# Kernel optimization log

Hardware: AMD Instinct MI355X
Metric: run time of the kernel (lower is better)

The kernel has to match this reference:

```python
import jax, jax.numpy as jnp
import numpy as np

B, S, D, H, L = 4, 2048, 512, 8, 4
DFF = 4 * D
CW = 128          # context_window
LS_MIN, LS_MAX = -6.0, 1.5


def setup_inputs() -> dict:
    key = jax.random.key(0)
    ks = jax.random.split(key, 10)
    s = 0.02
    p = lambda k, shape: jax.random.normal(k, shape, jnp.float32) * s
    return {
        "x": jax.random.normal(ks[0], (B, S, 2), jnp.float32),
        "W_in": p(ks[1], (D, 2)), "b_in": jnp.zeros((D,), jnp.float32),
        "pos": p(ks[2], (1, S, D)),
        "Wqkv": p(ks[3], (L, 3 * D, D)), "bqkv": jnp.zeros((L, 3 * D), jnp.float32),
        "Wo": p(ks[4], (L, D, D)), "bo": jnp.zeros((L, D), jnp.float32),
        "W1": p(ks[5], (L, DFF, D)), "b1": jnp.zeros((L, DFF), jnp.float32),
        "W2": p(ks[6], (L, D, DFF)), "b2": jnp.zeros((L, D), jnp.float32),
        "ln1_g": jnp.ones((L, D), jnp.float32), "ln1_b": jnp.zeros((L, D), jnp.float32),
        "ln2_g": jnp.ones((L, D), jnp.float32), "ln2_b": jnp.zeros((L, D), jnp.float32),
        "W_head": p(ks[7], (4, D)), "b_head": jnp.zeros((4,), jnp.float32),
    }


def _ln(x, g, b):
    m = x.mean(-1, keepdims=True)
    v = ((x - m) ** 2).mean(-1, keepdims=True)
    return (x - m) / jnp.sqrt(v + 1e-5) * g + b


def reference(x, W_in, b_in, pos, Wqkv, bqkv, Wo, bo, W1, b1, W2, b2,
              ln1_g, ln1_b, ln2_g, ln2_b, W_head, b_head):
    Bx, Sx, _ = x.shape
    h = x @ W_in.T + b_in + pos[:, :Sx, :]          # [B,S,D]
    idx = jnp.arange(Sx)
    # True = disallowed: future OR older than context window
    mask = (idx[None, :] > idx[:, None]) | (idx[None, :] < idx[:, None] - CW)
    dh = D // H
    scale = 1.0 / np.sqrt(dh).astype(np.float32)
    neg = jnp.float32(-1e30)
    for l in range(L):
        # self-attention (post-LN, as nn.TransformerEncoderLayer default)
        qkv = h @ Wqkv[l].T + bqkv[l]               # [B,S,3D]
        q, k, v = jnp.split(qkv, 3, axis=-1)
        q = q.reshape(Bx, Sx, H, dh)
        k = k.reshape(Bx, Sx, H, dh)
        v = v.reshape(Bx, Sx, H, dh)
        scores = jnp.einsum('bqhd,bkhd->bhqk', q, k) * scale
        scores = jnp.where(mask, neg, scores)
        attn = jax.nn.softmax(scores, axis=-1)
        o = jnp.einsum('bhqk,bkhd->bqhd', attn, v).reshape(Bx, Sx, D)
        h = _ln(h + o @ Wo[l].T + bo[l], ln1_g[l], ln1_b[l])
        # GELU FFN (exact erf gelu, torch default)
        ff = jax.nn.gelu(h @ W1[l].T + b1[l], approximate=False) @ W2[l].T + b2[l]
        h = _ln(h + ff, ln2_g[l], ln2_b[l])
    out = h @ W_head.T + b_head                     # [B,S,4]
    mu = out[..., :2]
    log_sigma = jnp.clip(out[..., 2:], LS_MIN, LS_MAX)
    return mu, log_sigma
```

## Files before the change

kernel.cpp:

```cpp
#include <hip/hip_runtime.h>
#include <hip/hip_bf16.h>
#include <math.h>

constexpr int Bc = 4;
constexpr int Sc = 2048;
constexpr int Dc = 512;
constexpr int Hc = 8;
constexpr int DHc = 64;
constexpr int Lc = 4;
constexpr int DFFc = 2048;
constexpr int Tc = Bc * Sc;
constexpr int QKVW = 3 * Dc;

typedef __attribute__((ext_vector_type(8))) short short8;
typedef __attribute__((ext_vector_type(4))) float f32x4;

static __device__ __forceinline__ float u16tof(unsigned int u) {
  return __uint_as_float(u << 16);
}
static __device__ __forceinline__ unsigned short ftobf(float f) {
  __hip_bfloat16 h = __float2bfloat16(f);
  return *reinterpret_cast<unsigned short*>(&h);
}
static __device__ __forceinline__ void gload_lds16(const void* g, void* l) {
  __builtin_amdgcn_global_load_lds(
      (const __attribute__((address_space(1))) void*)g,
      (__attribute__((address_space(3))) void*)l, 16, 0, 0);
}

static __device__ __forceinline__ int swzK(int row, int col) {
  return row * 64 + ((((col >> 3) ^ (row & 7)) << 3) | (col & 7));
}
static __device__ __forceinline__ int swzW(int row, int col) {
  return row * 192 + ((((col >> 3) ^ (row & 7)) << 3) | (col & 7));
}

__global__ __launch_bounds__(256) void k_f2bf(const float* __restrict__ in,
                                              unsigned short* __restrict__ out,
                                              int n) {
  int i = blockIdx.x * 256 + threadIdx.x;
  if (i < n) out[i] = ftobf(in[i]);
}

__global__ __launch_bounds__(256) void k_embed(const float* __restrict__ x,
                                               const float* __restrict__ W_in,
                                               const float* __restrict__ b_in,
                                               const float* __restrict__ pos,
                                               float* __restrict__ h,
                                               unsigned short* __restrict__ hb) {
  int idx = blockIdx.x * 256 + threadIdx.x;
  int t = idx >> 9;
  int d = idx & 511;
  int s = t & (Sc - 1);
  float v = x[t * 2 + 0] * W_in[d * 2 + 0] + x[t * 2 + 1] * W_in[d * 2 + 1] +
            b_in[d] + pos[(size_t)s * Dc + d];
  h[idx] = v;
  hb[idx] = ftobf(v);
}

template <int MODE, int OUTBF, int KK>
__global__ __launch_bounds__(256) void k_mgemm(const unsigned short* __restrict__ A,
                                               const unsigned short* __restrict__ W,
                                               const float* __restrict__ bias,
                                               const float* __restrict__ res,
                                               void* __restrict__ Cout,
                                               int M, int N) {
  constexpr int NSTEP = KK / 32;
  __shared__ short As[4][512 * 8];
  __shared__ short Bs[4][512 * 8];
  const int tid = threadIdx.x;
  const int lane = tid & 63;
  const int wid = tid >> 6;
  const int wm = wid >> 1;
  const int wn = wid & 1;

  const int nwg = gridDim.x * gridDim.y;
  const int bid = blockIdx.y * gridDim.x + blockIdx.x;
  const int swz = (bid & 7) * (nwg >> 3) + (bid >> 3);
  const int m0 = (swz / gridDim.x) * 128;
  const int n0 = (swz % gridDim.x) * 128;

  int r0S, c0S, r1S, c1S;
  {
    int p = tid;
    int rp = p >> 3, q = (p & 7) ^ (rp & 7);
    r0S = (rp << 1) | (q >> 2);
    c0S = q & 3;
    p = tid + 256;
    rp = p >> 3;
    q = (p & 7) ^ (rp & 7);
    r1S = (rp << 1) | (q >> 2);
    c1S = q & 3;
  }
  const unsigned short* a0p = A + (size_t)(m0 + r0S) * KK + c0S * 8;
  const unsigned short* a1p = A + (size_t)(m0 + r1S) * KK + c1S * 8;
  const unsigned short* b0p = W + (size_t)(n0 + r0S) * KK + c0S * 8;
  const unsigned short* b1p = W + (size_t)(n0 + r1S) * KK + c1S * 8;
  const int d0 = (tid & ~63) * 8;
  const int d1 = ((tid + 256) & ~63) * 8;

  f32x4 acc[4][4] = {};
  const int lr = lane & 15;
  const int chr = lane >> 4;

#pragma unroll
  for (int t = 0; t < 3; ++t) {
    const int ko = t * 32;
    gload_lds16(a0p + ko, &As[t][d0]);
    gload_lds16(a1p + ko, &As[t][d1]);
    gload_lds16(b0p + ko, &Bs[t][d0]);
    gload_lds16(b1p + ko, &Bs[t][d1]);
  }

#pragma unroll 4
  for (int s = 0; s < NSTEP; ++s) {
    if (s + 3 <= NSTEP)
      asm volatile("s_waitcnt vmcnt(8)" ::: "memory");
    else if (s + 2 <= NSTEP)
      asm volatile("s_waitcnt vmcnt(4)" ::: "memory");
    else
      asm volatile("s_waitcnt vmcnt(0)" ::: "memory");
    __builtin_amdgcn_s_barrier();
    __builtin_amdgcn_sched_barrier(0);

    if (s + 3 < NSTEP) {
      const int ko = (s + 3) * 32;
      const int nb = (s + 3) & 3;
      gload_lds16(a0p + ko, &As[nb][d0]);
      gload_lds16(a1p + ko, &As[nb][d1]);
      gload_lds16(b0p + ko, &Bs[nb][d0]);
      gload_lds16(b1p + ko, &Bs[nb][d1]);
    }

    const int buf = s & 3;
    short8 af[4], bfr[4];
#pragma unroll
    for (int mi = 0; mi < 4; ++mi) {
      int row = wm * 64 + mi * 16 + lr;
      int rp = row >> 1;
      int p = rp * 8 + (((((row & 1) << 2) | chr)) ^ (rp & 7));
      af[mi] = *(const short8*)&As[buf][p * 8];
    }
#pragma unroll
    for (int ni = 0; ni < 4; ++ni) {
      int row = wn * 64 + ni * 16 + lr;
      int rp = row >> 1;
      int p = rp * 8 + (((((row & 1) << 2) | chr)) ^ (rp & 7));
      bfr[ni] = *(const short8*)&Bs[buf][p * 8];
    }
    __builtin_amdgcn_s_setprio(1);
#pragma unroll
    for (int mi = 0; mi < 4; ++mi)
#pragma unroll
      for (int ni = 0; ni < 4; ++ni)
        acc[mi][ni] = __builtin_amdgcn_mfma_f32_16x16x32_bf16(
            af[mi], bfr[ni], acc[mi][ni], 0, 0, 0);
    __builtin_amdgcn_s_setprio(0);
  }

  const int cj = lane & 15;
  const int rj = (lane >> 4) * 4;
#pragma unroll
  for (int mi = 0; mi < 4; ++mi) {
#pragma unroll
    for (int ni = 0; ni < 4; ++ni) {
      int n = n0 + wn * 64 + ni * 16 + cj;
      float bn = bias[n];
#pragma unroll
      for (int j = 0; j < 4; ++j) {
        int m = m0 + wm * 64 + mi * 16 + rj + j;
        float v = acc[mi][ni][j] + bn;
        if (MODE == 1) v += res[(size_t)m * N + n];
        if (MODE == 2) v = 0.5f * v * (1.0f + erff(v * 0.70710678118654752f));
        if (OUTBF)
          ((unsigned short*)Cout)[(size_t)m * N + n] = ftobf(v);
        else
          ((float*)Cout)[(size_t)m * N + n] = v;
      }
    }
  }
}

__global__ __launch_bounds__(256) void k_attn(const unsigned short* __restrict__ qkv,
                                              unsigned short* __restrict__ o) {
  __shared__ unsigned short Ks[192 * 64];
  __shared__ unsigned short Vt[64 * 192];
  __shared__ unsigned short Ps[64 * 192];

  const int tid = threadIdx.x;
  const int lane = tid & 63;
  const int w = tid >> 6;
  const int idx = blockIdx.x;
  const int qb = idx & 31;
  const int hh = (idx >> 5) & 7;
  const int b = idx >> 8;
  const int q0 = qb * 64;
  const int kstart = max(0, q0 - 128);
  const int nk = q0 + 64 - kstart;

  for (int c = tid; c < nk * 8; c += 256) {
    int j = c >> 3, ch = c & 7;
    short8 kv = *(const short8*)&qkv[(size_t)(b * Sc + kstart + j) * QKVW + Dc + hh * DHc + ch * 8];
    *(short8*)&Ks[swzK(j, ch * 8)] = kv;
  }
  for (int c = tid; c < (nk >> 1) * 8; c += 256) {
    int jp = c >> 3, ch = c & 7;
    int j = jp * 2;
    const unsigned short* base =
        &qkv[(size_t)(b * Sc + kstart + j) * QKVW + 2 * Dc + hh * DHc + ch * 8];
    short8 v0 = *(const short8*)base;
    short8 v1 = *(const short8*)(base + QKVW);
#pragma unroll
    for (int i = 0; i < 8; ++i) {
      unsigned int pk = (unsigned short)v0[i] | ((unsigned int)(unsigned short)v1[i] << 16);
      *(unsigned int*)&Vt[swzW(ch * 8 + i, j)] = pk;
    }
  }
  if (nk < 192) {
    for (int c = tid; c < 64 * 64; c += 256) {
      int d = c >> 6, jo = c & 63;
      *(unsigned int*)&Vt[swzW(d, 64 + jo * 2)] = 0;
    }
  }

  const int qg = q0 + w * 16 + (lane & 15);
  const int kg8 = (lane >> 4) * 8;
  const unsigned short* qp = &qkv[(size_t)(b * Sc + qg) * QKVW + hh * DHc + kg8];
  short8 bq0 = *(const short8*)qp;
  short8 bq1 = *(const short8*)(qp + 32);
  __syncthreads();

  const int jb = max(0, q0 + w * 16 - 128) - kstart;

  f32x4 sacc[9];
#pragma unroll
  for (int t = 0; t < 9; ++t) {
    int key = jb + t * 16 + (lane & 15);
    short8 a0 = *(const short8*)&Ks[swzK(key, kg8)];
    short8 a1 = *(const short8*)&Ks[swzK(key, 32 + kg8)];
    f32x4 z = {0.f, 0.f, 0.f, 0.f};
    z = __builtin_amdgcn_mfma_f32_16x16x32_bf16(a0, bq0, z, 0, 0, 0);
    sacc[t] = __builtin_amdgcn_mfma_f32_16x16x32_bf16(a1, bq1, z, 0, 0, 0);
  }

  const int rj = (lane >> 4) * 4;
  float mx = -1e30f;
#pragma unroll
  for (int t = 0; t < 9; ++t) {
#pragma unroll
    for (int j = 0; j < 4; ++j) {
      int kglob = kstart + jb + t * 16 + rj + j;
      bool valid = (kglob <= qg) && (kglob + 128 >= qg);
      float s = valid ? sacc[t][j] * 0.125f : -1e30f;
      sacc[t][j] = s;
      mx = fmaxf(mx, s);
    }
  }
  mx = fmaxf(mx, __shfl_xor(mx, 16));
  mx = fmaxf(mx, __shfl_xor(mx, 32));
  float sum = 0.f;
#pragma unroll
  for (int t = 0; t < 9; ++t)
#pragma unroll
    for (int j = 0; j < 4; ++j) {
      float e = __expf(sacc[t][j] - mx);
      sacc[t][j] = e;
      sum += e;
    }
  sum += __shfl_xor(sum, 16);
  sum += __shfl_xor(sum, 32);
  const float inv = 1.0f / sum;

  const int prow = w * 16 + (lane & 15);
#pragma unroll
  for (int t = 0; t < 9; ++t) {
    int c0 = jb + t * 16 + rj;
    unsigned int p0 = ftobf(sacc[t][0] * inv) |
                      ((unsigned int)ftobf(sacc[t][1] * inv) << 16);
    unsigned int p1 = ftobf(sacc[t][2] * inv) |
                      ((unsigned int)ftobf(sacc[t][3] * inv) << 16);
    *(unsigned int*)&Ps[swzW(prow, c0)] = p0;
    *(unsigned int*)&Ps[swzW(prow, c0 + 2)] = p1;
  }
  {
    int g2 = (lane >> 4) * 2;
    for (int col = g2; col < jb; col += 8)
      *(unsigned int*)&Ps[swzW(prow, col)] = 0;
    for (int col = jb + 144 + g2; col < 192; col += 8)
      *(unsigned int*)&Ps[swzW(prow, col)] = 0;
  }
  f32x4 oacc[4] = {};
#pragma unroll
  for (int kb = 0; kb < 6; ++kb) {
    short8 pa = *(const short8*)&Ps[swzW(prow, kb * 32 + kg8)];
#pragma unroll
    for (int dt = 0; dt < 4; ++dt) {
      short8 vb = *(const short8*)&Vt[swzW(dt * 16 + (lane & 15), kb * 32 + kg8)];
      oacc[dt] = __builtin_amdgcn_mfma_f32_16x16x32_bf16(pa, vb, oacc[dt], 0, 0, 0);
    }
  }
  const int cj = lane & 15;
#pragma unroll
  for (int j = 0; j < 4; ++j)
#pragma unroll
    for (int dt = 0; dt < 4; ++dt)
      o[(size_t)(b * Sc + q0 + w * 16 + rj + j) * Dc + hh * DHc + dt * 16 + cj] =
          ftobf(oacc[dt][j]);
}

__global__ __launch_bounds__(256) void k_ln(const float* __restrict__ in,
                                            const float* __restrict__ g,
                                            const float* __restrict__ bta,
                                            float* __restrict__ out,
                                            unsigned short* __restrict__ outb) {
  const int wid = threadIdx.x >> 6;
  const int lane = threadIdx.x & 63;
  const int t = blockIdx.x * 4 + wid;
  const float* row = in + (size_t)t * Dc;
  float v[8];
  float sum = 0.0f, sq = 0.0f;
#pragma unroll
  for (int i = 0; i < 8; ++i) {
    float xv = row[lane + i * 64];
    v[i] = xv;
    sum += xv;
    sq += xv * xv;
  }
#pragma unroll
  for (int off = 32; off; off >>= 1) {
    sum += __shfl_xor(sum, off);
    sq += __shfl_xor(sq, off);
  }
  float m = sum * (1.0f / 512.0f);
  float var = sq * (1.0f / 512.0f) - m * m;
  float rstd = rsqrtf(var + 1e-5f);
#pragma unroll
  for (int i = 0; i < 8; ++i) {
    int d = lane + i * 64;
    float ov = (v[i] - m) * rstd * g[d] + bta[d];
    out[(size_t)t * Dc + d] = ov;
    outb[(size_t)t * Dc + d] = ftobf(ov);
  }
}

__global__ __launch_bounds__(256) void k_head(const float* __restrict__ h,
                                              const float* __restrict__ Wh,
                                              const float* __restrict__ bh,
                                              float* __restrict__ outp) {
  const int wid = threadIdx.x >> 6;
  const int lane = threadIdx.x & 63;
  const int t = blockIdx.x * 4 + wid;
  const float* row = h + (size_t)t * Dc;
  float a0 = 0, a1 = 0, a2 = 0, a3 = 0;
#pragma unroll
  for (int i = 0; i < 8; ++i) {
    int d = lane + i * 64;
    float xv = row[d];
    a0 += xv * Wh[0 * Dc + d];
    a1 += xv * Wh[1 * Dc + d];
    a2 += xv * Wh[2 * Dc + d];
    a3 += xv * Wh[3 * Dc + d];
  }
#pragma unroll
  for (int off = 32; off; off >>= 1) {
    a0 += __shfl_xor(a0, off);
    a1 += __shfl_xor(a1, off);
    a2 += __shfl_xor(a2, off);
    a3 += __shfl_xor(a3, off);
  }
  if (lane == 0) {
    outp[(size_t)t * 2 + 0] = a0 + bh[0];
    outp[(size_t)t * 2 + 1] = a1 + bh[1];
    outp[(size_t)Tc * 2 + (size_t)t * 2 + 0] = fminf(fmaxf(a2 + bh[2], -6.0f), 1.5f);
    outp[(size_t)Tc * 2 + (size_t)t * 2 + 1] = fminf(fmaxf(a3 + bh[3], -6.0f), 1.5f);
  }
}

extern "C" void kernel_launch(void* const* d_in, const int* in_sizes, int n_in,
                              void* d_out, int out_size, void* d_ws, size_t ws_size,
                              hipStream_t stream) {
  const float* x    = (const float*)d_in[0];
  const float* W_in = (const float*)d_in[1];
  const float* b_in = (const float*)d_in[2];
  const float* pos  = (const float*)d_in[3];
  const float* Wqkv = (const float*)d_in[4];
  const float* bqkv = (const float*)d_in[5];
  const float* Wo   = (const float*)d_in[6];
  const float* bo   = (const float*)d_in[7];
  const float* W1   = (const float*)d_in[8];
  const float* b1   = (const float*)d_in[9];
  const float* W2   = (const float*)d_in[10];
  const float* b2   = (const float*)d_in[11];
  const float* ln1g = (const float*)d_in[12];
  const float* ln1b = (const float*)d_in[13];
  const float* ln2g = (const float*)d_in[14];
  const float* ln2b = (const float*)d_in[15];
  const float* Wh   = (const float*)d_in[16];
  const float* bh   = (const float*)d_in[17];
  float* out = (float*)d_out;

  char* p = (char*)d_ws;
  float* h  = (float*)p;           p += (size_t)Tc * Dc * 4;
  float* t2 = (float*)p;           p += (size_t)Tc * Dc * 4;
  unsigned short* hb  = (unsigned short*)p; p += (size_t)Tc * Dc * 2;
  unsigned short* ob  = (unsigned short*)p; p += (size_t)Tc * Dc * 2;
  unsigned short* big = (unsigned short*)p; p += (size_t)Tc * DFFc * 2;
  unsigned short* wqb = (unsigned short*)p; p += (size_t)Lc * QKVW * Dc * 2;
  unsigned short* wob = (unsigned short*)p; p += (size_t)Lc * Dc * Dc * 2;
  unsigned short* w1b = (unsigned short*)p; p += (size_t)Lc * DFFc * Dc * 2;
  unsigned short* w2b = (unsigned short*)p; p += (size_t)Lc * Dc * DFFc * 2;

  k_f2bf<<<Lc * QKVW * Dc / 256, 256, 0, stream>>>(Wqkv, wqb, Lc * QKVW * Dc);
  k_f2bf<<<Lc * Dc * Dc / 256, 256, 0, stream>>>(Wo, wob, Lc * Dc * Dc);
  k_f2bf<<<Lc * DFFc * Dc / 256, 256, 0, stream>>>(W1, w1b, Lc * DFFc * Dc);
  k_f2bf<<<Lc * Dc * DFFc / 256, 256, 0, stream>>>(W2, w2b, Lc * Dc * DFFc);

  k_embed<<<(Tc * Dc) / 256, 256, 0, stream>>>(x, W_in, b_in, pos, h, hb);

  for (int l = 0; l < Lc; ++l) {
    const unsigned short* wq_l = wqb + (size_t)l * QKVW * Dc;
    const unsigned short* wo_l = wob + (size_t)l * Dc * Dc;
    const unsigned short* w1_l = w1b + (size_t)l * DFFc * Dc;
    const unsigned short* w2_l = w2b + (size_t)l * Dc * DFFc;

    k_mgemm<0, 1, Dc><<<dim3(QKVW / 128, Tc / 128), 256, 0, stream>>>(
        hb, wq_l, bqkv + (size_t)l * QKVW, nullptr, big, Tc, QKVW);

    k_attn<<<Bc * Hc * (Sc / 64), 256, 0, stream>>>(big, ob);

    k_mgemm<1, 0, Dc><<<dim3(Dc / 128, Tc / 128), 256, 0, stream>>>(
        ob, wo_l, bo + (size_t)l * Dc, h, t2, Tc, Dc);

    k_ln<<<Tc / 4, 256, 0, stream>>>(t2, ln1g + (size_t)l * Dc, ln1b + (size_t)l * Dc, h, hb);

    k_mgemm<2, 1, Dc><<<dim3(DFFc / 128, Tc / 128), 256, 0, stream>>>(
        hb, w1_l, b1 + (size_t)l * DFFc, nullptr, big, Tc, DFFc);

    k_mgemm<1, 0, DFFc><<<dim3(Dc / 128, Tc / 128), 256, 0, stream>>>(
        big, w2_l, b2 + (size_t)l * Dc, h, t2, Tc, Dc);

    k_ln<<<Tc / 4, 256, 0, stream>>>(t2, ln2g + (size_t)l * Dc, ln2b + (size_t)l * Dc, h, hb);
  }

  k_head<<<Tc / 4, 256, 0, stream>>>(h, Wh, bh, out);
}
```

Measured before the change: 670.2 us.

## Replace 4-wave 128x128 GEMM with single-wave 64x64 double-buffered GEMM

```diff
diff --git a/kernel.cpp b/kernel.cpp
--- a/kernel.cpp
+++ b/kernel.cpp
@@ -59,103 +59,86 @@
 }
 
 template <int MODE, int OUTBF, int KK>
-__global__ __launch_bounds__(256) void k_mgemm(const unsigned short* __restrict__ A,
-                                               const unsigned short* __restrict__ W,
-                                               const float* __restrict__ bias,
-                                               const float* __restrict__ res,
-                                               void* __restrict__ Cout,
-                                               int M, int N) {
+__global__ __launch_bounds__(64) void k_wgemm(const unsigned short* __restrict__ A,
+                                              const unsigned short* __restrict__ W,
+                                              const float* __restrict__ bias,
+                                              const float* __restrict__ res,
+                                              void* __restrict__ Cout,
+                                              int M, int N) {
   constexpr int NSTEP = KK / 32;
-  __shared__ short As[4][512 * 8];
-  __shared__ short Bs[4][512 * 8];
-  const int tid = threadIdx.x;
-  const int lane = tid & 63;
-  const int wid = tid >> 6;
-  const int wm = wid >> 1;
-  const int wn = wid & 1;
+  __shared__ unsigned short As[2][64 * 32];
+  __shared__ unsigned short Bs[2][64 * 32];
+  const int lane = threadIdx.x;
 
   const int nwg = gridDim.x * gridDim.y;
   const int bid = blockIdx.y * gridDim.x + blockIdx.x;
   const int swz = (bid & 7) * (nwg >> 3) + (bid >> 3);
-  const int m0 = (swz / gridDim.x) * 128;
-  const int n0 = (swz % gridDim.x) * 128;
-
-  int r0S, c0S, r1S, c1S;
-  {
-    int p = tid;
+  const int m0 = (swz / gridDim.x) * 64;
+  const int n0 = (swz % gridDim.x) * 64;
+
+  const unsigned short* Ap[4];
+  const unsigned short* Wp[4];
+#pragma unroll
+  for (int i = 0; i < 4; ++i) {
+    int p = i * 64 + lane;
     int rp = p >> 3, q = (p & 7) ^ (rp & 7);
-    r0S = (rp << 1) | (q >> 2);
-    c0S = q & 3;
-    p = tid + 256;
-    rp = p >> 3;
-    q = (p & 7) ^ (rp & 7);
-    r1S = (rp << 1) | (q >> 2);
-    c1S = q & 3;
-  }
-  const unsigned short* a0p = A + (size_t)(m0 + r0S) * KK + c0S * 8;
-  const unsigned short* a1p = A + (size_t)(m0 + r1S) * KK + c1S * 8;
-  const unsigned short* b0p = W + (size_t)(n0 + r0S) * KK + c0S * 8;
-  const unsigned short* b1p = W + (size_t)(n0 + r1S) * KK + c1S * 8;
-  const int d0 = (tid & ~63) * 8;
-  const int d1 = ((tid + 256) & ~63) * 8;
+    int row = (rp << 1) | (q >> 2);
+    int ch = q & 3;
+    Ap[i] = A + (size_t)(m0 + row) * KK + ch * 8;
+    Wp[i] = W + (size_t)(n0 + row) * KK + ch * 8;
+  }
 
   f32x4 acc[4][4] = {};
   const int lr = lane & 15;
   const int chr = lane >> 4;
 
 #pragma unroll
-  for (int t = 0; t < 3; ++t) {
-    const int ko = t * 32;
-    gload_lds16(a0p + ko, &As[t][d0]);
-    gload_lds16(a1p + ko, &As[t][d1]);
-    gload_lds16(b0p + ko, &Bs[t][d0]);
-    gload_lds16(b1p + ko, &Bs[t][d1]);
-  }
-
-#pragma unroll 4
+  for (int i = 0; i < 4; ++i) {
+    gload_lds16(Ap[i], &As[0][i * 512]);
+    gload_lds16(Wp[i], &Bs[0][i * 512]);
+  }
+
   for (int s = 0; s < NSTEP; ++s) {
-    if (s + 3 <= NSTEP)
+    const int buf = s & 1;
+    if (s + 1 < NSTEP) {
+      const int ko = (s + 1) * 32;
+      const int nb = buf ^ 1;
+#pragma unroll
+      for (int i = 0; i < 4; ++i) {
+        gload_lds16(Ap[i] + ko, &As[nb][i * 512]);
+        gload_lds16(Wp[i] + ko, &Bs[nb][i * 512]);
+      }
+      __builtin_amdgcn_sched_barrier(0);
       asm volatile("s_waitcnt vmcnt(8)" ::: "memory");
-    else if (s + 2 <= NSTEP)
-      asm volatile("s_waitcnt vmcnt(4)" ::: "memory");
-    else
+    } else {
+      __builtin_amdgcn_sched_barrier(0);
       asm volatile("s_waitcnt vmcnt(0)" ::: "memory");
-    __builtin_amdgcn_s_barrier();
+    }
     __builtin_amdgcn_sched_barrier(0);
 
-    if (s + 3 < NSTEP) {
-      const int ko = (s + 3) * 32;
-      const int nb = (s + 3) & 3;
-      gload_lds16(a0p + ko, &As[nb][d0]);
-      gload_lds16(a1p + ko, &As[nb][d1]);
-      gload_lds16(b0p + ko, &Bs[nb][d0]);
-      gload_lds16(b1p + ko, &Bs[nb][d1]);
-    }
-
-    const int buf = s & 3;
     short8 af[4], bfr[4];
 #pragma unroll
     for (int mi = 0; mi < 4; ++mi) {
-      int row = wm * 64 + mi * 16 + lr;
+      int row = mi * 16 + lr;
       int rp = row >> 1;
       int p = rp * 8 + (((((row & 1) << 2) | chr)) ^ (rp & 7));
       af[mi] = *(const short8*)&As[buf][p * 8];
     }
 #pragma unroll
     for (int ni = 0; ni < 4; ++ni) {
-      int row = wn * 64 + ni * 16 + lr;
+      int row = ni * 16 + lr;
       int rp = row >> 1;
       int p = rp * 8 + (((((row & 1) << 2) | chr)) ^ (rp & 7));
       bfr[ni] = *(const short8*)&Bs[buf][p * 8];
     }
-    __builtin_amdgcn_s_setprio(1);
+    asm volatile("s_waitcnt lgkmcnt(0)" ::: "memory");
+    __builtin_amdgcn_sched_barrier(0);
 #pragma unroll
     for (int mi = 0; mi < 4; ++mi)
 #pragma unroll
       for (int ni = 0; ni < 4; ++ni)
         acc[mi][ni] = __builtin_amdgcn_mfma_f32_16x16x32_bf16(
             af[mi], bfr[ni], acc[mi][ni], 0, 0, 0);
-    __builtin_amdgcn_s_setprio(0);
   }
 
   const int cj = lane & 15;
@@ -164,11 +147,11 @@
   for (int mi = 0; mi < 4; ++mi) {
 #pragma unroll
     for (int ni = 0; ni < 4; ++ni) {
-      int n = n0 + wn * 64 + ni * 16 + cj;
+      int n = n0 + ni * 16 + cj;
       float bn = bias[n];
 #pragma unroll
       for (int j = 0; j < 4; ++j) {
-        int m = m0 + wm * 64 + mi * 16 + rj + j;
+        int m = m0 + mi * 16 + rj + j;
         float v = acc[mi][ni][j] + bn;
         if (MODE == 1) v += res[(size_t)m * N + n];
         if (MODE == 2) v = 0.5f * v * (1.0f + erff(v * 0.70710678118654752f));
@@ -423,20 +406,20 @@
     const unsigned short* w1_l = w1b + (size_t)l * DFFc * Dc;
     const unsigned short* w2_l = w2b + (size_t)l * Dc * DFFc;
 
-    k_mgemm<0, 1, Dc><<<dim3(QKVW / 128, Tc / 128), 256, 0, stream>>>(
+    k_wgemm<0, 1, Dc><<<dim3(QKVW / 64, Tc / 64), 64, 0, stream>>>(
         hb, wq_l, bqkv + (size_t)l * QKVW, nullptr, big, Tc, QKVW);
 
     k_attn<<<Bc * Hc * (Sc / 64), 256, 0, stream>>>(big, ob);
 
-    k_mgemm<1, 0, Dc><<<dim3(Dc / 128, Tc / 128), 256, 0, stream>>>(
+    k_wgemm<1, 0, Dc><<<dim3(Dc / 64, Tc / 64), 64, 0, stream>>>(
         ob, wo_l, bo + (size_t)l * Dc, h, t2, Tc, Dc);
 
     k_ln<<<Tc / 4, 256, 0, stream>>>(t2, ln1g + (size_t)l * Dc, ln1b + (size_t)l * Dc, h, hb);
 
-    k_mgemm<2, 1, Dc><<<dim3(DFFc / 128, Tc / 128), 256, 0, stream>>>(
+    k_wgemm<2, 1, Dc><<<dim3(DFFc / 64, Tc / 64), 64, 0, stream>>>(
         hb, w1_l, b1 + (size_t)l * DFFc, nullptr, big, Tc, DFFc);
 
-    k_mgemm<1, 0, DFFc><<<dim3(Dc / 128, Tc / 128), 256, 0, stream>>>(
+    k_wgemm<1, 0, DFFc><<<dim3(Dc / 64, Tc / 64), 64, 0, stream>>>(
         big, w2_l, b2 + (size_t)l * Dc, h, t2, Tc, Dc);
 
     k_ln<<<Tc / 4, 256, 0, stream>>>(t2, ln2g + (size_t)l * Dc, ln2b + (size_t)l * Dc, h, hb);
```

Measured after the change: 743.1 us. 10.9% more time.
